# Kernel tuning notes

Hardware: AMD Instinct MI355X
Metric: run time of the kernel (lower is better)

## Reference

```python
import jax, jax.numpy as jnp
import numpy as np

NUM_HOPS = 8
SIGMA = 0.1
EPS = 1e-12  # torch F.normalize default eps


def _l2_normalize(x):
    # torch.nn.functional.normalize(x, dim=1): x / max(||x||_2, eps)
    norm = jnp.linalg.norm(x, axis=1, keepdims=True)
    return x / jnp.maximum(norm, EPS)


def setup_inputs() -> dict:
    key = jax.random.key(0)
    k1, k2 = jax.random.split(key)
    N, E, D = 100000, 3200000, 128
    x = jax.random.normal(k1, (N, D), dtype=jnp.float32)
    edge_index = jax.random.randint(k2, (2, E), 0, N, dtype=jnp.int64)
    return {"x": x, "edge_index": edge_index}


def reference(x, edge_index):
    # A[i, j] = 1 for each edge (i=src, j=dst); A^T @ h scatters h[src] into rows dst.
    # Duplicate edges coalesce by summation, matching torch sparse mm.
    N = x.shape[0]
    src = edge_index[0]
    dst = edge_index[1]
    noise_key = jax.random.key(42)
    cur = _l2_normalize(x)
    outs = [cur]
    for k in range(NUM_HOPS):
        aggr = jax.ops.segment_sum(cur[src], dst, num_segments=N)  # [N, D]
        noise = SIGMA * jax.random.normal(jax.random.fold_in(noise_key, k), aggr.shape, dtype=aggr.dtype)
        cur = _l2_normalize(aggr + noise)
        outs.append(cur)
    return jnp.stack(outs)  # [num_hops+1, N, D]
```

## Files before the change

kernel.cpp:

```cpp
#include <hip/hip_runtime.h>
#include <hip/hip_fp16.h>
#include <stdint.h>

#define D 128
#define NUM_HOPS 8
#define FILLA_EPT 16

typedef float f32x2 __attribute__((ext_vector_type(2)));
typedef float f32x4 __attribute__((ext_vector_type(4)));
typedef unsigned int u32x4 __attribute__((ext_vector_type(4)));

__host__ __device__ inline void tf2x32(uint32_t k0, uint32_t k1,
                                       uint32_t x0, uint32_t x1,
                                       uint32_t* o0, uint32_t* o1) {
  uint32_t ks2 = k0 ^ k1 ^ 0x1BD11BDAu;
  x0 += k0; x1 += k1;
#define TF_RND(r) { x0 += x1; x1 = (x1 << r) | (x1 >> (32 - r)); x1 ^= x0; }
  TF_RND(13) TF_RND(15) TF_RND(26) TF_RND(6)
  x0 += k1; x1 += ks2 + 1u;
  TF_RND(17) TF_RND(29) TF_RND(16) TF_RND(24)
  x0 += ks2; x1 += k0 + 2u;
  TF_RND(13) TF_RND(15) TF_RND(26) TF_RND(6)
  x0 += k0; x1 += k1 + 3u;
  TF_RND(17) TF_RND(29) TF_RND(16) TF_RND(24)
  x0 += k1; x1 += ks2 + 4u;
  TF_RND(13) TF_RND(15) TF_RND(26) TF_RND(6)
  x0 += ks2; x1 += k0 + 5u;
#undef TF_RND
  *o0 = x0; *o1 = x1;
}

__device__ inline float erfinv_f32(float x) {
  float w = -log1pf(-x * x);
  float p;
  if (w < 5.0f) {
    w = w - 2.5f;
    p = 2.81022636e-08f;
    p = fmaf(p, w, 3.43273939e-07f);
    p = fmaf(p, w, -3.5233877e-06f);
    p = fmaf(p, w, -4.39150654e-06f);
    p = fmaf(p, w, 0.00021858087f);
    p = fmaf(p, w, -0.00125372503f);
    p = fmaf(p, w, -0.00417768164f);
    p = fmaf(p, w, 0.246640727f);
    p = fmaf(p, w, 1.50140941f);
  } else {
    w = sqrtf(w) - 3.0f;
    p = -0.000200214257f;
    p = fmaf(p, w, 0.000100950558f);
    p = fmaf(p, w, 0.00134934322f);
    p = fmaf(p, w, -0.00367342844f);
    p = fmaf(p, w, 0.00573950773f);
    p = fmaf(p, w, -0.0076224613f);
    p = fmaf(p, w, 0.00943887047f);
    p = fmaf(p, w, 1.00167406f);
    p = fmaf(p, w, 2.83297682f);
  }
  return p * x;
}

__device__ inline float noise_from_bits(uint32_t bits) {
  const float lo = -0.99999994f;
  uint32_t fb = (bits >> 9) | 0x3f800000u;
  float f = __uint_as_float(fb) - 1.0f;
  float u = fmaxf(lo, fmaf(f, 2.0f, lo));
  return 0.1f * (1.41421354f * erfinv_f32(u));
}

__device__ inline float noise_elem(uint32_t fk0, uint32_t fk1, long t) {
  uint32_t o0, o1;
  tf2x32(fk0, fk1, (uint32_t)(((unsigned long)t) >> 32), (uint32_t)t, &o0, &o1);
  return noise_from_bits(o0 ^ o1);
}

__device__ inline bool edges_are_i64(const int* __restrict__ ei) {
  return (ei[1] | ei[3] | ei[5] | ei[7] | ei[9] | ei[11] | ei[13] | ei[15]) == 0;
}

__global__ __launch_bounds__(256) void zero256_kernel(int* __restrict__ p) {
  p[threadIdx.x] = 0;
}

__global__ __launch_bounds__(256) void bucket_hist_kernel(const int* __restrict__ ei,
                                                          int* __restrict__ bucketCount,
                                                          long E, int shift) {
  __shared__ int cnt[256];
  int tid = threadIdx.x;
  cnt[tid] = 0;
  __syncthreads();
  long base = (long)blockIdx.x * (256 * FILLA_EPT);
  bool i64 = edges_are_i64(ei);
  #pragma unroll
  for (int j = 0; j < FILLA_EPT; ++j) {
    long e = base + tid + (long)j * 256;
    if (e < E) {
      int d = __builtin_nontemporal_load(&ei[i64 ? (2 * (E + e)) : (E + e)]);
      atomicAdd(&cnt[d >> shift], 1);
    }
  }
  __syncthreads();
  if (cnt[tid] > 0) atomicAdd(&bucketCount[tid], cnt[tid]);
}

__global__ __launch_bounds__(256) void bucket_scan_kernel(const int* __restrict__ bucketCount,
                                                          int* __restrict__ bucketBase,
                                                          int* __restrict__ bucketCursor,
                                                          int nb, int E) {
  __shared__ int lds[256];
  int tid = threadIdx.x;
  int v = (tid < nb) ? bucketCount[tid] : 0;
  lds[tid] = v;
  __syncthreads();
  for (int off = 1; off < 256; off <<= 1) {
    int t = (tid >= off) ? lds[tid - off] : 0;
    __syncthreads();
    lds[tid] += t;
    __syncthreads();
  }
  int excl = lds[tid] - v;
  if (tid < nb) { bucketBase[tid] = excl; bucketCursor[tid] = excl; }
  if (tid == 0) bucketBase[nb] = E;
}

__global__ __launch_bounds__(256) void fillA_kernel(const int* __restrict__ ei,
                                                    int* __restrict__ bucketCursor,
                                                    uint64_t* __restrict__ tmp,
                                                    long E, int shift, int nb) {
  __shared__ int ldsCount[256];
  __shared__ int ldsBase[256];
  __shared__ int ldsRank[256];
  int tid = threadIdx.x;
  long base = (long)blockIdx.x * (256 * FILLA_EPT);
  bool i64 = edges_are_i64(ei);

  int sv[FILLA_EPT], dv[FILLA_EPT];
  ldsCount[tid] = 0; ldsRank[tid] = 0;
  __syncthreads();

  #pragma unroll
  for (int j = 0; j < FILLA_EPT; ++j) {
    long e = base + tid + (long)j * 256;
    if (e < E) {
      sv[j] = __builtin_nontemporal_load(&ei[i64 ? (2 * e) : e]);
      dv[j] = __builtin_nontemporal_load(&ei[i64 ? (2 * (E + e)) : (E + e)]);
      atomicAdd(&ldsCount[dv[j] >> shift], 1);
    } else { sv[j] = -1; dv[j] = -1; }
  }
  __syncthreads();
  if (tid < nb && ldsCount[tid] > 0)
    ldsBase[tid] = atomicAdd(&bucketCursor[tid], ldsCount[tid]);
  __syncthreads();
  #pragma unroll
  for (int j = 0; j < FILLA_EPT; ++j) {
    if (dv[j] >= 0) {
      int b = dv[j] >> shift;
      int r = atomicAdd(&ldsRank[b], 1);
      tmp[ldsBase[b] + r] = ((uint64_t)(uint32_t)dv[j] << 32) | (uint32_t)sv[j];
    }
  }
}

__global__ __launch_bounds__(256) void fillB3_kernel(const uint64_t* __restrict__ tmp,
                                                     const int* __restrict__ bucketBase,
                                                     int* __restrict__ row_ptr,
                                                     int* __restrict__ col,
                                                     int shift, int sb, int N, int nb) {
  __shared__ int h[4096];
  __shared__ int ps[256];
  int b = blockIdx.x;
  int tid = threadIdx.x;
  int r0 = b << shift;
  int bs = 1 << shift;
  int rows = N - r0; if (rows > bs) rows = bs;
  int beg = bucketBase[b], end = bucketBase[b + 1];
  int nkey = bs << 3;

  for (int i = tid; i < nkey; i += 256) h[i] = 0;
  __syncthreads();
  for (int i = beg + tid; i < end; i += 256) {
    uint64_t e = __builtin_nontemporal_load(&tmp[i]);
    int r = (int)(e >> 32) - r0;
    int band = (int)((uint32_t)e >> sb);
    atomicAdd(&h[(r << 3) | band], 1);
  }
  __syncthreads();
  int K = nkey >> 8;
  int base_i = tid * K;
  int sum = 0;
  for (int j = 0; j < K; ++j) sum += h[base_i + j];
  ps[tid] = sum;
  __syncthreads();
  for (int off = 1; off < 256; off <<= 1) {
    int t = (tid >= off) ? ps[tid - off] : 0;
    __syncthreads();
    ps[tid] += t;
    __syncthreads();
  }
  int run = ps[tid] - sum;
  for (int j = 0; j < K; ++j) {
    int c = h[base_i + j];
    h[base_i + j] = run;
    run += c;
  }
  __syncthreads();
  for (int r = tid; r < rows; r += 256) row_ptr[r0 + r] = beg + h[r << 3];
  if (b == nb - 1 && tid == 0) row_ptr[N] = end;
  __syncthreads();
  for (int i = beg + tid; i < end; i += 256) {
    uint64_t e = __builtin_nontemporal_load(&tmp[i]);
    int r = (int)(e >> 32) - r0;
    uint32_t s = (uint32_t)e;
    int slot = beg + atomicAdd(&h[(r << 3) | (s >> sb)], 1);
    col[slot] = (int)s;
  }
}

__global__ __launch_bounds__(256) void norm0_kernel(const float* __restrict__ in,
                                                    float* __restrict__ out,
                                                    __half* __restrict__ mir, int N) {
  long t = (long)blockIdx.x * blockDim.x + threadIdx.x;
  int row = (int)(t >> 6);
  int lane = (int)(t & 63);
  if (row >= N) return;
  float2 v = *(const float2*)(in + (size_t)row * D + lane * 2);
  float s = v.x * v.x + v.y * v.y;
  #pragma unroll
  for (int off = 32; off > 0; off >>= 1) s += __shfl_xor(s, off, 64);
  float inv = 1.0f / fmaxf(sqrtf(s), 1e-12f);
  f32x2 o; o.x = v.x * inv; o.y = v.y * inv;
  __builtin_nontemporal_store(o, (f32x2*)(out + (size_t)row * D + lane * 2));
  __half2 h = __float22half2_rn(make_float2(o.x, o.y));
  ((uint32_t*)mir)[(size_t)row * 64 + lane] = *(const uint32_t*)&h;
}

__global__ __launch_bounds__(256) void gather_hop_f16(const __half* __restrict__ mirIn,
                                                      float* __restrict__ nxt,
                                                      __half* __restrict__ mirOut,
                                                      const int* __restrict__ row_ptr,
                                                      const int* __restrict__ col,
                                                      int N, uint32_t fk0, uint32_t fk1) {
  long t = (long)blockIdx.x * blockDim.x + threadIdx.x;
  int row = (int)(t >> 6);
  if (row >= N) return;
  int lane = (int)(t & 63);
  int q = lane >> 4;
  int l16 = lane & 15;

  long t0 = (long)row * D + 2 * lane;
  float n0 = noise_elem(fk0, fk1, t0);
  float n1 = noise_elem(fk0, fk1, t0 + 1);

  float acc[8];
  #pragma unroll
  for (int j = 0; j < 8; ++j) acc[j] = 0.f;

  auto acc8 = [&](uint4 a) {
    const __half2* hp = (const __half2*)&a;
    #pragma unroll
    for (int j = 0; j < 4; ++j) {
      float2 f = __half22float2(hp[j]);
      acc[2 * j]     += f.x;
      acc[2 * j + 1] += f.y;
    }
  };

  const uint4* mir4 = (const uint4*)mirIn;
  int beg = row_ptr[row], end = row_ptr[row + 1];
  int i = beg + q;
  for (; i + 4 < end; i += 8) {
    int s0 = __builtin_nontemporal_load(&col[i]);
    int s1 = __builtin_nontemporal_load(&col[i + 4]);
    uint4 a = mir4[(size_t)s0 * 16 + l16];
    uint4 b = mir4[(size_t)s1 * 16 + l16];
    acc8(a); acc8(b);
  }
  for (; i < end; i += 4) {
    int s = __builtin_nontemporal_load(&col[i]);
    acc8(mir4[(size_t)s * 16 + l16]);
  }

  #pragma unroll
  for (int j = 0; j < 8; ++j) {
    acc[j] += __shfl_xor(acc[j], 16, 64);
    acc[j] += __shfl_xor(acc[j], 32, 64);
  }

  #pragma unroll
  for (int j = 0; j < 8; ++j) {
    int src = (l16 << 2) | (j >> 1);
    acc[j] += __shfl((j & 1) ? n1 : n0, src, 64);
  }

  float ss = 0.f;
  #pragma unroll
  for (int j = 0; j < 8; ++j) ss += acc[j] * acc[j];
  ss += __shfl_xor(ss, 1, 64);
  ss += __shfl_xor(ss, 2, 64);
  ss += __shfl_xor(ss, 4, 64);
  ss += __shfl_xor(ss, 8, 64);
  float inv = 1.0f / fmaxf(sqrtf(ss), 1e-12f);
  #pragma unroll
  for (int j = 0; j < 8; ++j) acc[j] *= inv;

  if (q == 0) {
    f32x4 o0 = {acc[0], acc[1], acc[2], acc[3]};
    f32x4 o1 = {acc[4], acc[5], acc[6], acc[7]};
    f32x4* op = (f32x4*)(nxt + (size_t)row * D + l16 * 8);
    __builtin_nontemporal_store(o0, op);
    __builtin_nontemporal_store(o1, op + 1);
  } else if (q == 1) {
    __half2 h0 = __float22half2_rn(make_float2(acc[0], acc[1]));
    __half2 h1 = __float22half2_rn(make_float2(acc[2], acc[3]));
    __half2 h2 = __float22half2_rn(make_float2(acc[4], acc[5]));
    __half2 h3 = __float22half2_rn(make_float2(acc[6], acc[7]));
    u32x4 u = { *(const uint32_t*)&h0, *(const uint32_t*)&h1,
                *(const uint32_t*)&h2, *(const uint32_t*)&h3 };
    __builtin_nontemporal_store(u, (u32x4*)mirOut + ((size_t)row * 16 + l16));
  }
}

__global__ __launch_bounds__(256) void noise_kernel(float* __restrict__ out,
                                                    uint32_t fk0, uint32_t fk1, long n) {
  long t = (long)blockIdx.x * blockDim.x + threadIdx.x;
  if (t >= n) return;
  out[t] = noise_elem(fk0, fk1, t);
}

__global__ __launch_bounds__(256) void scatter_kernel(const float* __restrict__ cur,
                                                      float* __restrict__ aggr,
                                                      const int* __restrict__ ei, long E) {
  long tid = (long)blockIdx.x * blockDim.x + threadIdx.x;
  long e = tid >> 5;
  if (e >= E) return;
  int lane = (int)(tid & 31);
  bool i64 = edges_are_i64(ei);
  int s = ei[i64 ? (2 * e) : e];
  int d = ei[i64 ? (2 * (E + e)) : (E + e)];
  float4 v = *(const float4*)(cur + (size_t)s * D + lane * 4);
  float* dp = aggr + (size_t)d * D + lane * 4;
  unsafeAtomicAdd(dp + 0, v.x);
  unsafeAtomicAdd(dp + 1, v.y);
  unsafeAtomicAdd(dp + 2, v.z);
  unsafeAtomicAdd(dp + 3, v.w);
}

__global__ __launch_bounds__(256) void norm_kernel(const float* __restrict__ in,
                                                   float* __restrict__ out, int N) {
  long t = (long)blockIdx.x * blockDim.x + threadIdx.x;
  int row = (int)(t >> 6);
  int lane = (int)(t & 63);
  if (row >= N) return;
  float2 v = *(const float2*)(in + (size_t)row * D + lane * 2);
  float s = v.x * v.x + v.y * v.y;
  #pragma unroll
  for (int off = 32; off > 0; off >>= 1) s += __shfl_xor(s, off, 64);
  float inv = 1.0f / fmaxf(sqrtf(s), 1e-12f);
  float2 o; o.x = v.x * inv; o.y = v.y * inv;
  *(float2*)(out + (size_t)row * D + lane * 2) = o;
}

static inline size_t align_up(size_t v, size_t a) { return (v + a - 1) & ~(a - 1); }

extern "C" void kernel_launch(void* const* d_in, const int* in_sizes, int n_in,
                              void* d_out, int out_size, void* d_ws, size_t ws_size,
                              hipStream_t stream) {
  const float* x = (const float*)d_in[0];
  const int* ei = (const int*)d_in[1];
  const long N = in_sizes[0] / D;
  const long E = in_sizes[1] / 2;
  float* out = (float*)d_out;
  const long ND = N * D;

  uint32_t fk0[NUM_HOPS], fk1[NUM_HOPS];
  for (int k = 0; k < NUM_HOPS; ++k)
    tf2x32(0u, 42u, 0u, (uint32_t)k, &fk0[k], &fk1[k]);

  int shift = 9;
  while ((((N + ((long)1 << shift) - 1) >> shift)) > 256) shift++;
  const int nb = (int)((N + ((long)1 << shift) - 1) >> shift);
  const int bs = 1 << shift;
  int sb = 0;
  while ((((long)N - 1) >> sb) > 7) sb++;

  uintptr_t base = (uintptr_t)d_ws;
  size_t off = 0;
  auto carve = [&](size_t bytes, size_t align) -> uintptr_t {
    off = align_up(off, align);
    uintptr_t p = base + off;
    off += bytes;
    return p;
  };
  int* row_ptr      = (int*)carve((size_t)(N + 1) * 4, 256);
  int* bucketCount  = (int*)carve(256 * 4, 256);
  int* bucketBase   = (int*)carve((size_t)(nb + 1) * 4, 256);
  int* bucketCursor = (int*)carve((size_t)nb * 4, 256);
  int* col          = (int*)carve((size_t)E * 4, 256);
  uint64_t* tmp     = (uint64_t*)carve((size_t)E * 8, 256);
  __half* mirA      = (__half*)carve((size_t)ND * 2, 256);
  __half* mirB      = (__half*)carve((size_t)ND * 2, 256);
  size_t need_full = off;

  long nthreads = N * 64;
  int ngrid = (int)((nthreads + 255) / 256);

  if (ws_size >= need_full && nb <= 256 && bs >= 32 && bs <= 512) {
    long epw = 256L * FILLA_EPT;
    int nblk = (int)((E + epw - 1) / epw);
    zero256_kernel<<<1, 256, 0, stream>>>(bucketCount);
    bucket_hist_kernel<<<nblk, 256, 0, stream>>>(ei, bucketCount, E, shift);
    bucket_scan_kernel<<<1, 256, 0, stream>>>(bucketCount, bucketBase, bucketCursor, nb, (int)E);
    fillA_kernel<<<nblk, 256, 0, stream>>>(ei, bucketCursor, tmp, E, shift, nb);
    fillB3_kernel<<<nb, 256, 0, stream>>>(tmp, bucketBase, row_ptr, col, shift, sb, (int)N, nb);

    norm0_kernel<<<ngrid, 256, 0, stream>>>(x, out, mirA, (int)N);
    for (int k = 0; k < NUM_HOPS; ++k) {
      float* nxt = out + (size_t)(k + 1) * ND;
      const __half* mi = (k & 1) ? mirB : mirA;
      __half* mo       = (k & 1) ? mirA : mirB;
      gather_hop_f16<<<ngrid, 256, 0, stream>>>(mi, nxt, mo, row_ptr, col,
                                                (int)N, fk0[k], fk1[k]);
    }
  } else {
    norm_kernel<<<ngrid, 256, 0, stream>>>(x, out, (int)N);
    for (int k = 0; k < NUM_HOPS; ++k) {
      const float* cur = out + (size_t)k * ND;
      float* nxt = out + (size_t)(k + 1) * ND;
      noise_kernel<<<(int)((ND + 255) / 256), 256, 0, stream>>>(nxt, fk0[k], fk1[k], ND);
      long sthreads = E * 32;
      scatter_kernel<<<(int)((sthreads + 255) / 256), 256, 0, stream>>>(cur, nxt, ei, E);
      norm_kernel<<<ngrid, 256, 0, stream>>>(nxt, nxt, (int)N);
    }
  }
}
```

Measured before the change: 1.145 ms.

## Gather per 32-row chunk with source-band ordering for cache locality

The CSR build now groups each 32-destination-row chunk's edges by source band (16 bands), then by row. Each wavefront processes one 32-row chunk and walks the bands in order, so concurrent source reads fall in a narrow address range and hit cache better. Accumulators for all 32 rows stay in registers, and noise, normalization and output are staged through LDS. The cost is 64 accumulator registers per lane, lower occupancy and parallelism (one wave per 32 rows), a larger boundary array, and serial per-row segment loops.

```diff
diff --git a/kernel.cpp b/kernel.cpp
--- a/kernel.cpp
+++ b/kernel.cpp
@@ -7,8 +7,6 @@
 #define FILLA_EPT 16
 
 typedef float f32x2 __attribute__((ext_vector_type(2)));
-typedef float f32x4 __attribute__((ext_vector_type(4)));
-typedef unsigned int u32x4 __attribute__((ext_vector_type(4)));
 
 __host__ __device__ inline void tf2x32(uint32_t k0, uint32_t k1,
                                        uint32_t x0, uint32_t x1,
@@ -160,34 +158,32 @@
   }
 }
 
-__global__ __launch_bounds__(256) void fillB3_kernel(const uint64_t* __restrict__ tmp,
+__global__ __launch_bounds__(256) void fillB4_kernel(const uint64_t* __restrict__ tmp,
                                                      const int* __restrict__ bucketBase,
-                                                     int* __restrict__ row_ptr,
+                                                     int* __restrict__ bnd,
                                                      int* __restrict__ col,
-                                                     int shift, int sb, int N, int nb) {
-  __shared__ int h[4096];
+                                                     int sb, int N, int nb, int NC) {
+  __shared__ int h[8192];
   __shared__ int ps[256];
   int b = blockIdx.x;
   int tid = threadIdx.x;
-  int r0 = b << shift;
-  int bs = 1 << shift;
-  int rows = N - r0; if (rows > bs) rows = bs;
+  int r0 = b << 9;
   int beg = bucketBase[b], end = bucketBase[b + 1];
-  int nkey = bs << 3;
-
-  for (int i = tid; i < nkey; i += 256) h[i] = 0;
+
+  for (int i = tid; i < 8192; i += 256) h[i] = 0;
   __syncthreads();
   for (int i = beg + tid; i < end; i += 256) {
     uint64_t e = __builtin_nontemporal_load(&tmp[i]);
     int r = (int)(e >> 32) - r0;
-    int band = (int)((uint32_t)e >> sb);
-    atomicAdd(&h[(r << 3) | band], 1);
-  }
-  __syncthreads();
-  int K = nkey >> 8;
-  int base_i = tid * K;
+    uint32_t s = (uint32_t)e;
+    int key = ((r >> 5) << 9) | ((int)(s >> sb) << 5) | (r & 31);
+    atomicAdd(&h[key], 1);
+  }
+  __syncthreads();
+  int base_i = tid * 32;
   int sum = 0;
-  for (int j = 0; j < K; ++j) sum += h[base_i + j];
+  #pragma unroll
+  for (int j = 0; j < 32; ++j) sum += h[base_i + j];
   ps[tid] = sum;
   __syncthreads();
   for (int off = 1; off < 256; off <<= 1) {
@@ -197,20 +193,18 @@
     __syncthreads();
   }
   int run = ps[tid] - sum;
-  for (int j = 0; j < K; ++j) {
-    int c = h[base_i + j];
-    h[base_i + j] = run;
-    run += c;
-  }
-  __syncthreads();
-  for (int r = tid; r < rows; r += 256) row_ptr[r0 + r] = beg + h[r << 3];
-  if (b == nb - 1 && tid == 0) row_ptr[N] = end;
+  #pragma unroll
+  for (int j = 0; j < 32; ++j) { int c = h[base_i + j]; h[base_i + j] = run; run += c; }
+  __syncthreads();
+  for (int i = tid; i < 8192; i += 256) bnd[(size_t)b * 8192 + i] = beg + h[i];
+  if (b == nb - 1 && tid == 0) bnd[(size_t)NC * 512] = end;
   __syncthreads();
   for (int i = beg + tid; i < end; i += 256) {
     uint64_t e = __builtin_nontemporal_load(&tmp[i]);
     int r = (int)(e >> 32) - r0;
     uint32_t s = (uint32_t)e;
-    int slot = beg + atomicAdd(&h[(r << 3) | (s >> sb)], 1);
+    int key = ((r >> 5) << 9) | ((int)(s >> sb) << 5) | (r & 31);
+    int slot = beg + atomicAdd(&h[key], 1);
     col[slot] = (int)s;
   }
 }
@@ -233,89 +227,72 @@
   ((uint32_t*)mir)[(size_t)row * 64 + lane] = *(const uint32_t*)&h;
 }
 
-__global__ __launch_bounds__(256) void gather_hop_f16(const __half* __restrict__ mirIn,
-                                                      float* __restrict__ nxt,
-                                                      __half* __restrict__ mirOut,
-                                                      const int* __restrict__ row_ptr,
-                                                      const int* __restrict__ col,
-                                                      int N, uint32_t fk0, uint32_t fk1) {
-  long t = (long)blockIdx.x * blockDim.x + threadIdx.x;
-  int row = (int)(t >> 6);
-  if (row >= N) return;
-  int lane = (int)(t & 63);
-  int q = lane >> 4;
-  int l16 = lane & 15;
-
-  long t0 = (long)row * D + 2 * lane;
-  float n0 = noise_elem(fk0, fk1, t0);
-  float n1 = noise_elem(fk0, fk1, t0 + 1);
-
-  float acc[8];
-  #pragma unroll
-  for (int j = 0; j < 8; ++j) acc[j] = 0.f;
-
-  auto acc8 = [&](uint4 a) {
-    const __half2* hp = (const __half2*)&a;
+__global__ __launch_bounds__(256) void gather_band(const __half* __restrict__ mirIn,
+                                                   float* __restrict__ nxt,
+                                                   __half* __restrict__ mirOut,
+                                                   const int* __restrict__ bnd,
+                                                   const int* __restrict__ col,
+                                                   int NC, uint32_t fk0, uint32_t fk1) {
+  __shared__ float2 stage[4][16][64];
+  int wl = threadIdx.x >> 6;
+  int lane = threadIdx.x & 63;
+  int c = blockIdx.x * 4 + wl;
+  if (c >= NC) return;
+  const int* bc = bnd + (size_t)c * 512;
+  const uint32_t* mir32 = (const uint32_t*)mirIn;
+
+  float2 acc[32];
+  #pragma unroll
+  for (int r = 0; r < 32; ++r) { acc[r].x = 0.f; acc[r].y = 0.f; }
+
+  int cur = bc[0];
+  for (int b = 0; b < 16; ++b) {
     #pragma unroll
-    for (int j = 0; j < 4; ++j) {
-      float2 f = __half22float2(hp[j]);
-      acc[2 * j]     += f.x;
-      acc[2 * j + 1] += f.y;
-    }
-  };
-
-  const uint4* mir4 = (const uint4*)mirIn;
-  int beg = row_ptr[row], end = row_ptr[row + 1];
-  int i = beg + q;
-  for (; i + 4 < end; i += 8) {
-    int s0 = __builtin_nontemporal_load(&col[i]);
-    int s1 = __builtin_nontemporal_load(&col[i + 4]);
-    uint4 a = mir4[(size_t)s0 * 16 + l16];
-    uint4 b = mir4[(size_t)s1 * 16 + l16];
-    acc8(a); acc8(b);
-  }
-  for (; i < end; i += 4) {
-    int s = __builtin_nontemporal_load(&col[i]);
-    acc8(mir4[(size_t)s * 16 + l16]);
-  }
-
-  #pragma unroll
-  for (int j = 0; j < 8; ++j) {
-    acc[j] += __shfl_xor(acc[j], 16, 64);
-    acc[j] += __shfl_xor(acc[j], 32, 64);
-  }
-
-  #pragma unroll
-  for (int j = 0; j < 8; ++j) {
-    int src = (l16 << 2) | (j >> 1);
-    acc[j] += __shfl((j & 1) ? n1 : n0, src, 64);
-  }
-
-  float ss = 0.f;
-  #pragma unroll
-  for (int j = 0; j < 8; ++j) ss += acc[j] * acc[j];
-  ss += __shfl_xor(ss, 1, 64);
-  ss += __shfl_xor(ss, 2, 64);
-  ss += __shfl_xor(ss, 4, 64);
-  ss += __shfl_xor(ss, 8, 64);
-  float inv = 1.0f / fmaxf(sqrtf(ss), 1e-12f);
-  #pragma unroll
-  for (int j = 0; j < 8; ++j) acc[j] *= inv;
-
-  if (q == 0) {
-    f32x4 o0 = {acc[0], acc[1], acc[2], acc[3]};
-    f32x4 o1 = {acc[4], acc[5], acc[6], acc[7]};
-    f32x4* op = (f32x4*)(nxt + (size_t)row * D + l16 * 8);
-    __builtin_nontemporal_store(o0, op);
-    __builtin_nontemporal_store(o1, op + 1);
-  } else if (q == 1) {
-    __half2 h0 = __float22half2_rn(make_float2(acc[0], acc[1]));
-    __half2 h1 = __float22half2_rn(make_float2(acc[2], acc[3]));
-    __half2 h2 = __float22half2_rn(make_float2(acc[4], acc[5]));
-    __half2 h3 = __float22half2_rn(make_float2(acc[6], acc[7]));
-    u32x4 u = { *(const uint32_t*)&h0, *(const uint32_t*)&h1,
-                *(const uint32_t*)&h2, *(const uint32_t*)&h3 };
-    __builtin_nontemporal_store(u, (u32x4*)mirOut + ((size_t)row * 16 + l16));
+    for (int r = 0; r < 32; ++r) {
+      int seg_end = bc[b * 32 + r + 1];
+      int i = cur;
+      for (; i + 1 < seg_end; i += 2) {
+        int s0 = col[i], s1 = col[i + 1];
+        uint32_t u0 = mir32[(size_t)s0 * 64 + lane];
+        uint32_t u1 = mir32[(size_t)s1 * 64 + lane];
+        float2 f0 = __half22float2(*(const __half2*)&u0);
+        float2 f1 = __half22float2(*(const __half2*)&u1);
+        acc[r].x += f0.x + f1.x;
+        acc[r].y += f0.y + f1.y;
+      }
+      if (i < seg_end) {
+        int s0 = col[i];
+        uint32_t u0 = mir32[(size_t)s0 * 64 + lane];
+        float2 f0 = __half22float2(*(const __half2*)&u0);
+        acc[r].x += f0.x;
+        acc[r].y += f0.y;
+      }
+      cur = seg_end;
+    }
+  }
+
+  long rowBase = (long)c * 32;
+  #pragma unroll
+  for (int ph = 0; ph < 2; ++ph) {
+    #pragma unroll
+    for (int r = 0; r < 16; ++r) stage[wl][r][lane] = acc[ph * 16 + r];
+    for (int r = 0; r < 16; ++r) {
+      float2 a = stage[wl][r][lane];
+      long row = rowBase + ph * 16 + r;
+      long t0 = row * D + 2 * lane;
+      float a0 = a.x + noise_elem(fk0, fk1, t0);
+      float a1 = a.y + noise_elem(fk0, fk1, t0 + 1);
+      float ss = a0 * a0 + a1 * a1;
+      #pragma unroll
+      for (int off = 32; off > 0; off >>= 1) ss += __shfl_xor(ss, off, 64);
+      float inv = 1.0f / fmaxf(sqrtf(ss), 1e-12f);
+      a0 *= inv; a1 *= inv;
+      f32x2 o; o.x = a0; o.y = a1;
+      __builtin_nontemporal_store(o, (f32x2*)(nxt + row * D + 2 * lane));
+      __half2 h = __float22half2_rn(make_float2(a0, a1));
+      __builtin_nontemporal_store(*(const uint32_t*)&h,
+                                  (uint32_t*)mirOut + row * 64 + lane);
+    }
   }
 }
 
@@ -378,9 +355,9 @@
   int shift = 9;
   while ((((N + ((long)1 << shift) - 1) >> shift)) > 256) shift++;
   const int nb = (int)((N + ((long)1 << shift) - 1) >> shift);
-  const int bs = 1 << shift;
   int sb = 0;
-  while ((((long)N - 1) >> sb) > 7) sb++;
+  while ((((long)N - 1) >> sb) > 15) sb++;
+  const int NC = (int)(N / 32);
 
   uintptr_t base = (uintptr_t)d_ws;
   size_t off = 0;
@@ -390,10 +367,10 @@
     off += bytes;
     return p;
   };
-  int* row_ptr      = (int*)carve((size_t)(N + 1) * 4, 256);
   int* bucketCount  = (int*)carve(256 * 4, 256);
   int* bucketBase   = (int*)carve((size_t)(nb + 1) * 4, 256);
   int* bucketCursor = (int*)carve((size_t)nb * 4, 256);
+  int* bnd          = (int*)carve(((size_t)nb * 8192 + 1) * 4, 256);
   int* col          = (int*)carve((size_t)E * 4, 256);
   uint64_t* tmp     = (uint64_t*)carve((size_t)E * 8, 256);
   __half* mirA      = (__half*)carve((size_t)ND * 2, 256);
@@ -403,22 +380,23 @@
   long nthreads = N * 64;
   int ngrid = (int)((nthreads + 255) / 256);
 
-  if (ws_size >= need_full && nb <= 256 && bs >= 32 && bs <= 512) {
+  if (ws_size >= need_full && shift == 9 && nb <= 256 && (N % 32) == 0) {
     long epw = 256L * FILLA_EPT;
     int nblk = (int)((E + epw - 1) / epw);
     zero256_kernel<<<1, 256, 0, stream>>>(bucketCount);
     bucket_hist_kernel<<<nblk, 256, 0, stream>>>(ei, bucketCount, E, shift);
     bucket_scan_kernel<<<1, 256, 0, stream>>>(bucketCount, bucketBase, bucketCursor, nb, (int)E);
     fillA_kernel<<<nblk, 256, 0, stream>>>(ei, bucketCursor, tmp, E, shift, nb);
-    fillB3_kernel<<<nb, 256, 0, stream>>>(tmp, bucketBase, row_ptr, col, shift, sb, (int)N, nb);
+    fillB4_kernel<<<nb, 256, 0, stream>>>(tmp, bucketBase, bnd, col, sb, (int)N, nb, NC);
 
     norm0_kernel<<<ngrid, 256, 0, stream>>>(x, out, mirA, (int)N);
+    int ggrid = (NC + 3) / 4;
     for (int k = 0; k < NUM_HOPS; ++k) {
       float* nxt = out + (size_t)(k + 1) * ND;
       const __half* mi = (k & 1) ? mirB : mirA;
       __half* mo       = (k & 1) ? mirA : mirB;
-      gather_hop_f16<<<ngrid, 256, 0, stream>>>(mi, nxt, mo, row_ptr, col,
-                                                (int)N, fk0[k], fk1[k]);
+      gather_band<<<ggrid, 256, 0, stream>>>(mi, nxt, mo, bnd, col,
+                                             NC, fk0[k], fk1[k]);
     }
   } else {
     norm_kernel<<<ngrid, 256, 0, stream>>>(x, out, (int)N);
```

Result: slower. 4.420 ms (+286.1%).
